# Kernel optimization log

Hardware: AMD Instinct MI355X
Metric: run time of the kernel (lower is better)

Reference implementation:

```python
import jax, jax.numpy as jnp
import numpy as np

N_QUBITS = 8
N_LAYERS = 2
BATCH = 16384
INPUT_DIM = 3072
NUM_CLASSES = 10

I2 = np.eye(2, dtype=np.complex64)
PAULIS = [
    I2,
    np.array([[0, 1], [1, 0]], np.complex64),      # X
    np.array([[0, -1j], [1j, 0]], np.complex64),   # Y
    np.array([[1, 0], [0, -1]], np.complex64),     # Z
]
XX = np.kron(PAULIS[1], PAULIS[1])
YY = np.kron(PAULIS[2], PAULIS[2])
ZZ = np.kron(PAULIS[3], PAULIS[3])
I4 = np.eye(4, dtype=np.complex64)


def u3(p):
    # PennyLane U3(theta, phi, lambda)
    th, ph, lam = p[0], p[1], p[2]
    c = jnp.cos(th / 2).astype(jnp.complex64)
    s = jnp.sin(th / 2).astype(jnp.complex64)
    return jnp.stack([
        jnp.stack([c, -jnp.exp(1j * lam) * s]),
        jnp.stack([jnp.exp(1j * ph) * s, jnp.exp(1j * (ph + lam)) * c]),
    ])


def cu3(p):
    U = u3(p)
    Z = jnp.zeros((2, 2), U.dtype)
    Ic = jnp.asarray(I2)
    top = jnp.concatenate([Ic, Z], axis=1)
    bot = jnp.concatenate([Z, U], axis=1)
    return jnp.concatenate([top, bot], axis=0)


def ising(P, phi):
    # exp(-i phi/2 * P) with P a 2-qubit Pauli word (P^2 = I)
    return jnp.cos(phi / 2) * I4 - 1j * jnp.sin(phi / 2) * P


def apply_1q(psi, U, w):
    psi = jnp.moveaxis(psi, 1 + w, -1)
    psi = jnp.einsum('ij,...j->...i', U, psi)
    return jnp.moveaxis(psi, -1, 1 + w)


def apply_2q(psi, U, a, b):
    psi = jnp.moveaxis(psi, (1 + a, 1 + b), (-2, -1))
    sh = psi.shape
    psi = jnp.einsum('ij,...j->...i', U, psi.reshape(sh[:-2] + (4,)))
    return jnp.moveaxis(psi.reshape(sh), (-2, -1), (1 + a, 1 + b))


def apply_ry_batched(psi, theta, w):
    # per-sample RY angle (AngleEmbedding, rotation='Y')
    c = jnp.cos(theta / 2).reshape((-1,) + (1,) * (psi.ndim - 2))
    s = jnp.sin(theta / 2).reshape((-1,) + (1,) * (psi.ndim - 2))
    psi = jnp.moveaxis(psi, 1 + w, -1)
    a0, a1 = psi[..., 0], psi[..., 1]
    psi = jnp.stack([c * a0 - s * a1, s * a0 + c * a1], axis=-1)
    return jnp.moveaxis(psi, -1, 1 + w)


def dilated_conv(psi, W, wires):
    n = len(wires)
    if n == 8:
        pairs = [(0, 2), (1, 3), (4, 6), (5, 7)]
    elif n == 4:
        pairs = [(0, 2), (1, 3)]
    elif n == 2:
        pairs = [(0, 1)]
    else:
        pairs = [(i, i + 2) for i in range(n - 2)]
    processed = set()
    for q1, q2 in pairs:
        if q1 in wires and q2 in wires:
            psi = apply_1q(psi, u3(W[q1, 0:3]), q1)
            psi = apply_1q(psi, u3(W[q2, 3:6]), q2)
            psi = apply_2q(psi, ising(ZZ, W[q1, 6]), q1, q2)
            psi = apply_2q(psi, ising(YY, W[q1, 7]), q1, q2)
            psi = apply_2q(psi, ising(XX, W[q1, 8]), q1, q2)
            psi = apply_1q(psi, u3(W[q1, 9:12]), q1)
            psi = apply_1q(psi, u3(W[q2, 12:15]), q2)
            processed.update((q1, q2))
    for w in wires:
        if w not in processed:
            for i in range(5):
                psi = apply_1q(psi, u3(W[w, 3 * i:3 * i + 3]), w)
    return psi


def pooling(psi, P, wires):
    for indx, w in enumerate(wires):
        if indx % 2 == 1:
            # measure wire w, cond-U3 on wires[indx-1]; deferred -> CU3(ctrl=w, tgt=wires[indx-1])
            psi = apply_2q(psi, cu3(P[indx // 2]), w, wires[indx - 1])
    return psi


def _gray_pauli_words(k):
    # matches pennylane _n_k_gray_code(4, k) ordering, identity word dropped
    words = []
    for i in range(4 ** k):
        br = []
        v = i
        for _ in range(k):
            br.append(v % 4)
            v //= 4
        cw = [0] * k
        shift = 0
        for j in reversed(range(k)):
            cw[j] = (br[j] + shift) % 4
            shift += 4 - cw[j]
        if any(cw):
            words.append(tuple(cw))
    return words


def arbitrary_unitary(psi, weights, wires):
    # qml.ArbitraryUnitary: sequence of PauliRot(weights[i], word) gates
    k = len(wires)
    Ik = np.eye(2 ** k, dtype=np.complex64)
    for idx, cw in enumerate(_gray_pauli_words(k)):
        P = np.array([[1.0]], np.complex64)
        for p in cw:
            P = np.kron(P, PAULIS[p])
        th = weights[idx]
        G = jnp.cos(th / 2) * Ik - 1j * jnp.sin(th / 2) * P
        psi = apply_2q(psi, G, wires[0], wires[1])
    return psi


def run_circuit(features, conv, pool, last):
    B = features.shape[0]
    psi = jnp.zeros((B, 2 ** N_QUBITS), jnp.complex64).at[:, 0].set(1.0)
    psi = psi.reshape((B,) + (2,) * N_QUBITS)
    for w in range(N_QUBITS):
        psi = apply_ry_batched(psi, features[:, w], w)
    wires = list(range(N_QUBITS))
    for layer in range(N_LAYERS):
        psi = dilated_conv(psi, conv[layer], wires)
        psi = pooling(psi, pool[layer], wires)
        wires = wires[::2]
    psi = arbitrary_unitary(psi, last, wires)
    probs = psi.real ** 2 + psi.imag ** 2
    z0 = probs[:, 0].reshape(B, -1).sum(-1) - probs[:, 1].reshape(B, -1).sum(-1)
    return z0  # <Z_0> per sample


def setup_inputs():
    key = jax.random.key(0)
    ks = jax.random.split(key, 8)
    return {
        'x': jax.random.normal(ks[0], (BATCH, INPUT_DIM), jnp.float32),
        'fc_w': jax.random.normal(ks[1], (N_QUBITS, INPUT_DIM), jnp.float32) * 0.02,
        'fc_b': jnp.zeros((N_QUBITS,), jnp.float32),
        'conv_params': jax.random.normal(ks[2], (N_LAYERS, N_QUBITS, 15), jnp.float32),
        'pool_params': jax.random.normal(ks[3], (N_LAYERS, N_QUBITS // 2, 3), jnp.float32),
        'last_params': jax.random.normal(ks[4], (15,), jnp.float32),
        'fc_out_w': jax.random.normal(ks[5], (NUM_CLASSES, 1), jnp.float32),
        'fc_out_b': jnp.zeros((NUM_CLASSES,), jnp.float32),
    }


def reference(x, fc_w, fc_b, conv_params, pool_params, last_params, fc_out_w, fc_out_b):
    reduced = jnp.tanh(x @ fc_w.T + fc_b)                      # (B, n_qubits)
    z0 = run_circuit(reduced, conv_params, pool_params, last_params)  # (B,)
    logits = z0[:, None] * fc_out_w[:, 0][None, :] + fc_out_b  # (B, num_classes)
    return logits
```

## Files before the change

### kernel.cpp

```cpp
#include <hip/hip_runtime.h>
#include <math.h>

__device__ inline float2 cmul(float2 a, float2 b){
  return make_float2(a.x*b.x - a.y*b.y, a.x*b.y + a.y*b.x);
}
__device__ inline void cfma(float2& acc, float2 a, float2 b){
  acc.x += a.x*b.x - a.y*b.y;
  acc.y += a.x*b.y + a.y*b.x;
}

__device__ inline void mk_u3(const float* p, float2& u00, float2& u01, float2& u10, float2& u11){
  float s, c;   sincosf(0.5f*p[0], &s, &c);
  float sl, cl; sincosf(p[1], &sl, &cl);
  float sm, cm; sincosf(p[2], &sm, &cm);
  float s2, c2; sincosf(p[1] + p[2], &s2, &c2);
  u00 = make_float2(c, 0.f);
  u01 = make_float2(-s*cm, -s*sm);
  u10 = make_float2( s*cl,  s*sl);
  u11 = make_float2( c*c2,  c*s2);
}

__device__ inline void pauli2(int t, float2* m){
  if (t == 0){ m[0]=make_float2(1,0); m[1]=make_float2(0,0);  m[2]=make_float2(0,0); m[3]=make_float2(1,0); }
  else if (t == 1){ m[0]=make_float2(0,0); m[1]=make_float2(1,0);  m[2]=make_float2(1,0); m[3]=make_float2(0,0); }
  else if (t == 2){ m[0]=make_float2(0,0); m[1]=make_float2(0,-1); m[2]=make_float2(0,1); m[3]=make_float2(0,0); }
  else            { m[0]=make_float2(1,0); m[1]=make_float2(0,0);  m[2]=make_float2(0,0); m[3]=make_float2(-1,0);}
}

struct GSpec { int type; int w1; int w2; int poff; };
#define NG 66
__device__ const GSpec gspec[NG] = {
  {0,0,0,  0},{0,2,0, 33},{1,0,2,  6},{2,0,2,  7},{3,0,2,  8},{0,0,0,  9},{0,2,0, 42},
  {0,1,0, 15},{0,3,0, 48},{1,1,3, 21},{2,1,3, 22},{3,1,3, 23},{0,1,0, 24},{0,3,0, 57},
  {0,4,0, 60},{0,6,0, 93},{1,4,6, 66},{2,4,6, 67},{3,4,6, 68},{0,4,0, 69},{0,6,0,102},
  {0,5,0, 75},{0,7,0,108},{1,5,7, 81},{2,5,7, 82},{3,5,7, 83},{0,5,0, 84},{0,7,0,117},
  {4,1,0,1000},{4,3,2,1003},{4,5,4,1006},{4,7,6,1009},
  {0,0,0,120},{0,2,0,153},{1,0,2,126},{2,0,2,127},{3,0,2,128},{0,0,0,129},{0,2,0,162},
  {0,4,0,180},{0,4,0,183},{0,4,0,186},{0,4,0,189},{0,4,0,192},
  {0,6,0,210},{0,6,0,213},{0,6,0,216},{0,6,0,219},{0,6,0,222},
  {4,2,0,1012},{4,6,4,1015},
  {5,1,0,2000},{5,2,0,2001},{5,3,0,2002},{5,3,1,2003},{5,0,1,2004},
  {5,1,1,2005},{5,2,1,2006},{5,2,2,2007},{5,3,2,2008},{5,0,2,2009},
  {5,1,2,2010},{5,1,3,2011},{5,2,3,2012},{5,3,3,2013},{5,0,3,2014},
};

__device__ inline void apply1q(float2* S, int lane, int bit,
                               float2 u00, float2 u01, float2 u10, float2 u11){
  #pragma unroll
  for (int t = 0; t < 2; t++){
    int p  = lane + 64*t;
    int k0 = ((p >> bit) << (bit+1)) | (p & ((1<<bit)-1));
    int k1 = k0 | (1 << bit);
    float2 a = S[k0], b = S[k1];
    float2 na = make_float2(u00.x*a.x - u00.y*a.y + u01.x*b.x - u01.y*b.y,
                            u00.x*a.y + u00.y*a.x + u01.x*b.y + u01.y*b.x);
    float2 nb = make_float2(u10.x*a.x - u10.y*a.y + u11.x*b.x - u11.y*b.y,
                            u10.x*a.y + u10.y*a.x + u11.x*b.y + u11.y*b.x);
    S[k0] = na; S[k1] = nb;
  }
  __syncthreads();
}

__device__ inline void apply2q(float2* S, int lane, int bitA, int bitB, const float2* G){
  int hi = bitA > bitB ? bitA : bitB;
  int lo = bitA ^ bitB ^ hi;
  int t2  = ((lane >> lo) << (lo+1)) | (lane & ((1<<lo)-1));
  int k00 = ((t2   >> hi) << (hi+1)) | (t2   & ((1<<hi)-1));
  int mA = 1 << bitA, mB = 1 << bitB;
  int id[4] = { k00, k00|mB, k00|mA, k00|mA|mB };
  float2 v[4];
  #pragma unroll
  for (int r = 0; r < 4; r++) v[r] = S[id[r]];
  #pragma unroll
  for (int r = 0; r < 4; r++){
    float re = 0.f, im = 0.f;
    #pragma unroll
    for (int c = 0; c < 4; c++){
      float2 g = G[r*4 + c];
      re += g.x*v[c].x - g.y*v[c].y;
      im += g.x*v[c].y + g.y*v[c].x;
    }
    S[id[r]] = make_float2(re, im);
  }
  __syncthreads();
}

__global__ __launch_bounds__(64) void kern_sim(const float* __restrict__ conv,
                                               const float* __restrict__ pool,
                                               const float* __restrict__ last,
                                               float2* __restrict__ U){
  __shared__ float2 Gt[NG*16];
  __shared__ float2 Ft[14*16];
  __shared__ float2 Ms[7*16];
  __shared__ float2 S[256];
  const int lane = threadIdx.x;
  const int j = blockIdx.x;

  for (int g = lane; g < NG; g += 64){
    GSpec sp = gspec[g];
    const float* base;
    if (sp.poff >= 2000)      base = last + (sp.poff - 2000);
    else if (sp.poff >= 1000) base = pool + (sp.poff - 1000);
    else                      base = conv + sp.poff;
    float2 G[16];
    #pragma unroll
    for (int i = 0; i < 16; i++) G[i] = make_float2(0.f, 0.f);
    if (sp.type == 0){
      float2 a,b,c,d; mk_u3(base,a,b,c,d);
      G[0]=a; G[1]=b; G[2]=c; G[3]=d;
    } else if (sp.type == 1){
      float s,co; sincosf(0.5f*base[0], &s, &co);
      G[0]=make_float2(co,-s); G[5]=make_float2(co,s); G[10]=make_float2(co,s); G[15]=make_float2(co,-s);
    } else if (sp.type == 2){
      float s,co; sincosf(0.5f*base[0], &s, &co);
      G[0]=G[5]=G[10]=G[15]=make_float2(co,0.f);
      G[3]=make_float2(0.f,s); G[6]=make_float2(0.f,-s); G[9]=make_float2(0.f,-s); G[12]=make_float2(0.f,s);
    } else if (sp.type == 3){
      float s,co; sincosf(0.5f*base[0], &s, &co);
      G[0]=G[5]=G[10]=G[15]=make_float2(co,0.f);
      G[3]=G[6]=G[9]=G[12]=make_float2(0.f,-s);
    } else if (sp.type == 4){
      float2 a,b,c,d; mk_u3(base,a,b,c,d);
      G[0]=make_float2(1.f,0.f); G[5]=make_float2(1.f,0.f);
      G[10]=a; G[11]=b; G[14]=c; G[15]=d;
    } else {
      float s,co; sincosf(0.5f*base[0], &s, &co);
      float2 A2[4], B2[4]; pauli2(sp.w1,A2); pauli2(sp.w2,B2);
      #pragma unroll
      for (int i1 = 0; i1 < 2; i1++)
      #pragma unroll
      for (int i2 = 0; i2 < 2; i2++)
      #pragma unroll
      for (int j1 = 0; j1 < 2; j1++)
      #pragma unroll
      for (int j2 = 0; j2 < 2; j2++){
        float2 Pv = cmul(A2[i1*2+j1], B2[i2*2+j2]);
        int rr = i1*2+i2, cc = j1*2+j2;
        G[rr*4+cc] = make_float2((rr==cc ? co : 0.f) + s*Pv.y, -s*Pv.x);
      }
    }
    #pragma unroll
    for (int i = 0; i < 16; i++) Gt[g*16 + i] = G[i];
  }
  __syncthreads();

  const int fe = lane & 15;
  const int fr = fe >> 2, fc = fe & 3;

  {
    const int p  = lane >> 4;
    const int gb = p*7;
    float2 va = Gt[gb*16     + (fr>>1)*2 + (fc>>1)];
    float2 vb = Gt[(gb+1)*16 + (fr&1)*2  + (fc&1)];
    Ms[p*16 + fe] = cmul(va, vb);
    __syncthreads();
    for (int s = 0; s < 3; s++){
      float2 acc = make_float2(0.f, 0.f);
      #pragma unroll
      for (int k = 0; k < 4; k++)
        cfma(acc, Gt[(gb+2+s)*16 + fr*4 + k], Ms[p*16 + k*4 + fc]);
      __syncthreads();
      Ms[p*16 + fe] = acc;
      __syncthreads();
    }
    float2 ka = Gt[(gb+5)*16 + (fr>>1)*2 + (fc>>1)];
    float2 kb = Gt[(gb+6)*16 + (fr&1)*2  + (fc&1)];
    Ft[p*16 + fe] = cmul(ka, kb);
    __syncthreads();
    float2 acc = make_float2(0.f, 0.f);
    #pragma unroll
    for (int k = 0; k < 4; k++)
      cfma(acc, Ft[p*16 + fr*4 + k], Ms[p*16 + k*4 + fc]);
    __syncthreads();
    Ft[p*16 + fe] = acc;
    __syncthreads();
  }

  {
    const int grp = lane >> 4;
    if (grp == 0){
      float2 va = Gt[32*16 + (fr>>1)*2 + (fc>>1)];
      float2 vb = Gt[33*16 + (fr&1)*2  + (fc&1)];
      Ms[4*16 + fe] = cmul(va, vb);
    } else if (grp == 1){
      Ms[5*16 + fe] = Gt[51*16 + fe];
    } else if (lane < 40){
      int t = (lane-32)>>2, e2 = (lane-32)&3;
      Ms[6*16 + t*4 + e2] = Gt[(39+5*t)*16 + e2];
    }
    __syncthreads();
    for (int s = 1; s <= 14; s++){
      float2 val = make_float2(0.f, 0.f);
      int wf = 0, dst = 0;
      if (grp == 0){
        if (s <= 3){
          #pragma unroll
          for (int k = 0; k < 4; k++)
            cfma(val, Gt[(33+s)*16 + fr*4 + k], Ms[4*16 + k*4 + fc]);
          wf = 1; dst = 4*16 + fe;
        } else if (s == 4){
          float2 ka = Gt[37*16 + (fr>>1)*2 + (fc>>1)];
          float2 kb = Gt[38*16 + (fr&1)*2  + (fc&1)];
          val = cmul(ka, kb); wf = 1; dst = 0*16 + fe;
        } else if (s == 5){
          #pragma unroll
          for (int k = 0; k < 4; k++)
            cfma(val, Ms[0*16 + fr*4 + k], Ms[4*16 + k*4 + fc]);
          wf = 2; dst = 4*16 + fe;
        }
      } else if (grp == 1){
        #pragma unroll
        for (int k = 0; k < 4; k++)
          cfma(val, Gt[(51+s)*16 + fr*4 + k], Ms[5*16 + k*4 + fc]);
        if (s == 14){ wf = 2; dst = 13*16 + fe; }
        else        { wf = 1; dst = 5*16 + fe; }
      } else if (lane < 40 && s <= 4){
        int t = (lane-32)>>2, e2 = (lane-32)&3, r2 = e2>>1, c2 = e2&1;
        #pragma unroll
        for (int k = 0; k < 2; k++)
          cfma(val, Gt[(39+5*t+s)*16 + r2*2 + k], Ms[6*16 + t*4 + k*2 + c2]);
        if (s == 4){ wf = 2; dst = (5+t)*16 + e2; }
        else       { wf = 1; dst = 6*16 + t*4 + e2; }
      }
      __syncthreads();
      if (wf == 1) Ms[dst] = val;
      else if (wf == 2) Ft[dst] = val;
      __syncthreads();
    }
    for (int idx = lane; idx < 96; idx += 64){
      int q = idx >> 4, e = idx & 15;
      int gid = (q < 4) ? (28+q) : (q == 4 ? 49 : 50);
      Ft[(7+q)*16 + e] = Gt[gid*16 + e];
    }
  }
  __syncthreads();

  #pragma unroll
  for (int t = 0; t < 4; t++){ int k = lane + 64*t; S[k] = make_float2(k==j ? 1.f : 0.f, 0.f); }
  __syncthreads();

  apply2q(S, lane, 7, 5, &Ft[0*16]);
  apply2q(S, lane, 6, 4, &Ft[1*16]);
  apply2q(S, lane, 3, 1, &Ft[2*16]);
  apply2q(S, lane, 2, 0, &Ft[3*16]);
  apply2q(S, lane, 6, 7, &Ft[7*16]);
  apply2q(S, lane, 4, 5, &Ft[8*16]);
  apply2q(S, lane, 2, 3, &Ft[9*16]);
  apply2q(S, lane, 0, 1, &Ft[10*16]);
  apply2q(S, lane, 7, 5, &Ft[4*16]);
  apply1q(S, lane, 3, Ft[5*16+0], Ft[5*16+1], Ft[5*16+2], Ft[5*16+3]);
  apply1q(S, lane, 1, Ft[6*16+0], Ft[6*16+1], Ft[6*16+2], Ft[6*16+3]);
  apply2q(S, lane, 5, 7, &Ft[11*16]);
  apply2q(S, lane, 1, 3, &Ft[12*16]);
  apply2q(S, lane, 7, 3, &Ft[13*16]);

  #pragma unroll
  for (int t = 0; t < 4; t++){ int k = lane + 64*t; U[k*256 + j] = S[k]; }
}

__global__ __launch_bounds__(256) void kern_m2(const float2* __restrict__ U,
                                               float* __restrict__ mt){
  __shared__ float dsh[256];
  const int xm = blockIdx.x, i = threadIdx.x;
  const int j2 = i ^ xm;
  float acc = 0.f;
  #pragma unroll 4
  for (int k = 0; k < 128; k++){
    float2 ui0 = U[k*256 + i];
    float2 uj0 = U[k*256 + j2];
    float2 ui1 = U[(k+128)*256 + i];
    float2 uj1 = U[(k+128)*256 + j2];
    acc += (ui0.x*uj0.x + ui0.y*uj0.y) - (ui1.x*uj1.x + ui1.y*uj1.y);
  }
  dsh[i] = acc;
  __syncthreads();
  for (int bit = 1; bit < 256; bit <<= 1){
    float mine = dsh[i], other = dsh[i ^ bit];
    __syncthreads();
    dsh[i] = (i & bit) ? (other - mine) : (mine + other);
    __syncthreads();
  }
  if ((i & xm) == 0){
    int idx = 0, pw = 1;
    #pragma unroll
    for (int b2 = 0; b2 < 8; b2++){
      int dg = ((xm >> b2) & 1) ? 1 : (((i >> b2) & 1) ? 2 : 0);
      idx += dg * pw; pw *= 3;
    }
    mt[idx] = dsh[i] * (1.0f/256.0f);
  }
}

__global__ __launch_bounds__(256) void kern_gemv(const float* __restrict__ x,
                                                 const float* __restrict__ w,
                                                 const float* __restrict__ b,
                                                 float* __restrict__ red){
  __shared__ float4 wl[1536];
  const int tid = threadIdx.x;
  const int wave = tid >> 6, lane = tid & 63;
  const int rl = lane >> 5, co = lane & 31;
  const int row0 = blockIdx.x*16 + wave*4 + rl*2;
  const float4* xp0 = (const float4*)(x + (size_t)row0*3072);
  const float4* xp1 = (const float4*)(x + (size_t)(row0+1)*3072);
  const float4* wp  = (const float4*)w;
  float accA[8], accB[8];
  #pragma unroll
  for (int q = 0; q < 8; q++){ accA[q] = 0.f; accB[q] = 0.f; }

  for (int qt = 0; qt < 4; qt++){
    __syncthreads();
    #pragma unroll
    for (int i = 0; i < 6; i++){
      int idx = tid + 256*i;
      int q = idx / 192, cc = idx - q*192;
      wl[idx] = wp[q*768 + qt*192 + cc];
    }
    __syncthreads();
    #pragma unroll
    for (int it = 0; it < 6; it++){
      int cl = it*32 + co;
      float4 xa = xp0[qt*192 + cl];
      float4 xb = xp1[qt*192 + cl];
      #pragma unroll
      for (int q = 0; q < 8; q++){
        float4 wv = wl[q*192 + cl];
        accA[q] += wv.x*xa.x + wv.y*xa.y + wv.z*xa.z + wv.w*xa.w;
        accB[q] += wv.x*xb.x + wv.y*xb.y + wv.z*xb.z + wv.w*xb.w;
      }
    }
  }

  #pragma unroll
  for (int q = 0; q < 8; q++){
    float va = accA[q], vb = accB[q];
    va += __shfl_xor(va, 1);  vb += __shfl_xor(vb, 1);
    va += __shfl_xor(va, 2);  vb += __shfl_xor(vb, 2);
    va += __shfl_xor(va, 4);  vb += __shfl_xor(vb, 4);
    va += __shfl_xor(va, 8);  vb += __shfl_xor(vb, 8);
    va += __shfl_xor(va, 16); vb += __shfl_xor(vb, 16);
    accA[q] = va; accB[q] = vb;
  }
  if (co == 0){
    float4 a0 = make_float4(tanhf(accA[0]+b[0]), tanhf(accA[1]+b[1]),
                            tanhf(accA[2]+b[2]), tanhf(accA[3]+b[3]));
    float4 a1 = make_float4(tanhf(accA[4]+b[4]), tanhf(accA[5]+b[5]),
                            tanhf(accA[6]+b[6]), tanhf(accA[7]+b[7]));
    float4* rpA = (float4*)(red + (size_t)row0*8);
    rpA[0] = a0; rpA[1] = a1;
    float4 b0 = make_float4(tanhf(accB[0]+b[0]), tanhf(accB[1]+b[1]),
                            tanhf(accB[2]+b[2]), tanhf(accB[3]+b[3]));
    float4 b1 = make_float4(tanhf(accB[4]+b[4]), tanhf(accB[5]+b[5]),
                            tanhf(accB[6]+b[6]), tanhf(accB[7]+b[7]));
    float4* rpB = (float4*)(red + (size_t)(row0+1)*8);
    rpB[0] = b0; rpB[1] = b1;
  }
}

__global__ __launch_bounds__(256) void kern_contract(const float* __restrict__ red,
                                                     const float* __restrict__ mt,
                                                     const float* __restrict__ fow,
                                                     const float* __restrict__ fob,
                                                     float* __restrict__ out){
  __shared__ float mtl[9*27*32];
  __shared__ float zsh[4*64];
  const int tid = threadIdx.x;
  for (int idx = tid; idx < 9*27*32; idx += 256){
    int h  = idx / 864;
    int r  = idx - h*864;
    int mm = r >> 5, l = r & 31;
    mtl[idx] = (l < 27) ? mt[h*729 + mm*27 + l] : 0.f;
  }
  const int wave = tid >> 6, lane = tid & 63;
  const int e = blockIdx.x*64 + lane;
  const float4* rp = (const float4*)(red + (size_t)e*8);
  float4 r0 = rp[0], r1 = rp[1];
  __syncthreads();

  float rr[8] = {r0.x, r0.y, r0.z, r0.w, r1.x, r1.y, r1.z, r1.w};
  float sn[8], cs[8];
  #pragma unroll
  for (int q = 0; q < 8; q++) sincosf(rr[q], &sn[q], &cs[q]);
  float f0[3] = {1.f, sn[7], cs[7]};
  float f1[3] = {1.f, sn[6], cs[6]};
  float f2[3] = {1.f, sn[5], cs[5]};
  float g27[32];
  #pragma unroll
  for (int z = 27; z < 32; z++) g27[z] = 0.f;
  #pragma unroll
  for (int d2 = 0; d2 < 3; d2++)
  #pragma unroll
  for (int d1 = 0; d1 < 3; d1++)
  #pragma unroll
  for (int d0 = 0; d0 < 3; d0++)
    g27[9*d2 + 3*d1 + d0] = f2[d2]*f1[d1]*f0[d0];
  float4 glo4[8];
  #pragma unroll
  for (int v = 0; v < 8; v++)
    glo4[v] = make_float4(g27[4*v], g27[4*v+1], g27[4*v+2], g27[4*v+3]);
  float f3[3] = {1.f, sn[4], cs[4]};
  float f4[3] = {1.f, sn[3], cs[3]};
  float f5[3] = {1.f, sn[2], cs[2]};
  float gmid[27];
  #pragma unroll
  for (int d5 = 0; d5 < 3; d5++)
  #pragma unroll
  for (int d4 = 0; d4 < 3; d4++)
  #pragma unroll
  for (int d3 = 0; d3 < 3; d3++)
    gmid[9*d5 + 3*d4 + d3] = f5[d5]*f4[d4]*f3[d3];
  float f6[3] = {1.f, sn[1], cs[1]};
  float f7[3] = {1.f, sn[0], cs[0]};
  float ghi[9];
  #pragma unroll
  for (int d7 = 0; d7 < 3; d7++)
  #pragma unroll
  for (int d6 = 0; d6 < 3; d6++)
    ghi[3*d7 + d6] = f7[d7]*f6[d6];

  const int hbeg = (wave==0) ? 0 : (wave==1) ? 3 : (wave==2) ? 5 : 7;
  const int hend = hbeg + ((wave==0) ? 3 : 2);
  float part = 0.f;
  for (int h = hbeg; h < hend; h++){
    float ha = 0.f, hb = 0.f;
    #pragma unroll 3
    for (int mm = 0; mm < 27; mm++){
      const float4* mp = (const float4*)&mtl[(h*27 + mm) << 5];
      float d0 = 0.f, d1 = 0.f;
      #pragma unroll
      for (int v = 0; v < 8; v += 2){
        float4 m0 = mp[v], m1 = mp[v+1];
        d0 += m0.x*glo4[v].x   + m0.y*glo4[v].y   + m0.z*glo4[v].z   + m0.w*glo4[v].w;
        d1 += m1.x*glo4[v+1].x + m1.y*glo4[v+1].y + m1.z*glo4[v+1].z + m1.w*glo4[v+1].w;
      }
      float term = (d0 + d1) * gmid[mm];
      if (mm & 1) hb += term; else ha += term;
    }
    part += (ha + hb) * ghi[h];
  }
  zsh[wave*64 + lane] = part;
  __syncthreads();

  for (int idx = tid; idx < 640; idx += 256){
    int el = idx / 10, c = idx - el*10;
    float z = zsh[el] + zsh[64+el] + zsh[128+el] + zsh[192+el];
    out[((size_t)blockIdx.x*64 + el)*10 + c] = z*fow[c] + fob[c];
  }
}

extern "C" void kernel_launch(void* const* d_in, const int* in_sizes, int n_in,
                              void* d_out, int out_size, void* d_ws, size_t ws_size,
                              hipStream_t stream) {
  (void)in_sizes; (void)n_in; (void)out_size; (void)ws_size;
  const float* x    = (const float*)d_in[0];
  const float* fcw  = (const float*)d_in[1];
  const float* fcb  = (const float*)d_in[2];
  const float* conv = (const float*)d_in[3];
  const float* pool = (const float*)d_in[4];
  const float* last = (const float*)d_in[5];
  const float* fow  = (const float*)d_in[6];
  const float* fob  = (const float*)d_in[7];
  float* out = (float*)d_out;

  char* ws = (char*)d_ws;
  float2* U   = (float2*)ws;
  float*  red = (float*) (ws + 512*1024);
  float*  mt  = (float*) (ws + 1024*1024);

  kern_sim     <<<256,  64,  0, stream>>>(conv, pool, last, U);
  kern_m2      <<<256,  256, 0, stream>>>(U, mt);
  kern_gemv    <<<1024, 256, 0, stream>>>(x, fcw, fcb, red);
  kern_contract<<<256,  256, 0, stream>>>(red, mt, fow, fob, out);
}
```

Baseline: 355.8 us.

## Fuse circuit simulation into GEMV launch and pad mt layout in global memory

Merges the GEMV kernel and the unitary-simulation kernel into one launch. Blocks 0-1023 run the FC reduction and blocks 1024+ simulate circuit columns with 256 threads, the extra threads idling during gate application. kern_m2 now writes the moment tensor directly in the padded 32-stride layout and zeroes the padding. kern_contract then reads it straight from global/L2 instead of staging it in shared memory. The intent is to remove one launch, overlap the small sim work with the bandwidth-bound GEMV, and cut the per-block shared-memory staging in the contraction. The cost is that the sim blocks become less efficient and the contraction loads go through the cache.

```diff
diff --git a/kernel.cpp b/kernel.cpp
--- a/kernel.cpp
+++ b/kernel.cpp
@@ -44,11 +44,10 @@
   {5,1,2,2010},{5,1,3,2011},{5,2,3,2012},{5,3,3,2013},{5,0,3,2014},
 };
 
-__device__ inline void apply1q(float2* S, int lane, int bit,
-                               float2 u00, float2 u01, float2 u10, float2 u11){
-  #pragma unroll
-  for (int t = 0; t < 2; t++){
-    int p  = lane + 64*t;
+__device__ inline void apply1q_b(float2* S, int tid, int bit,
+                                 float2 u00, float2 u01, float2 u10, float2 u11){
+  if (tid < 128){
+    int p  = tid;
     int k0 = ((p >> bit) << (bit+1)) | (p & ((1<<bit)-1));
     int k1 = k0 | (1 << bit);
     float2 a = S[k0], b = S[k1];
@@ -61,42 +60,113 @@
   __syncthreads();
 }
 
-__device__ inline void apply2q(float2* S, int lane, int bitA, int bitB, const float2* G){
-  int hi = bitA > bitB ? bitA : bitB;
-  int lo = bitA ^ bitB ^ hi;
-  int t2  = ((lane >> lo) << (lo+1)) | (lane & ((1<<lo)-1));
-  int k00 = ((t2   >> hi) << (hi+1)) | (t2   & ((1<<hi)-1));
-  int mA = 1 << bitA, mB = 1 << bitB;
-  int id[4] = { k00, k00|mB, k00|mA, k00|mA|mB };
-  float2 v[4];
-  #pragma unroll
-  for (int r = 0; r < 4; r++) v[r] = S[id[r]];
-  #pragma unroll
-  for (int r = 0; r < 4; r++){
-    float re = 0.f, im = 0.f;
-    #pragma unroll
-    for (int c = 0; c < 4; c++){
-      float2 g = G[r*4 + c];
-      re += g.x*v[c].x - g.y*v[c].y;
-      im += g.x*v[c].y + g.y*v[c].x;
-    }
-    S[id[r]] = make_float2(re, im);
-  }
-  __syncthreads();
-}
-
-__global__ __launch_bounds__(64) void kern_sim(const float* __restrict__ conv,
-                                               const float* __restrict__ pool,
-                                               const float* __restrict__ last,
-                                               float2* __restrict__ U){
-  __shared__ float2 Gt[NG*16];
-  __shared__ float2 Ft[14*16];
-  __shared__ float2 Ms[7*16];
-  __shared__ float2 S[256];
-  const int lane = threadIdx.x;
-  const int j = blockIdx.x;
-
-  for (int g = lane; g < NG; g += 64){
+__device__ inline void apply2q_b(float2* S, int tid, int bitA, int bitB, const float2* G){
+  if (tid < 64){
+    int lane = tid;
+    int hi = bitA > bitB ? bitA : bitB;
+    int lo = bitA ^ bitB ^ hi;
+    int t2  = ((lane >> lo) << (lo+1)) | (lane & ((1<<lo)-1));
+    int k00 = ((t2   >> hi) << (hi+1)) | (t2   & ((1<<hi)-1));
+    int mA = 1 << bitA, mB = 1 << bitB;
+    int id[4] = { k00, k00|mB, k00|mA, k00|mA|mB };
+    float2 v[4];
+    #pragma unroll
+    for (int r = 0; r < 4; r++) v[r] = S[id[r]];
+    #pragma unroll
+    for (int r = 0; r < 4; r++){
+      float re = 0.f, im = 0.f;
+      #pragma unroll
+      for (int c = 0; c < 4; c++){
+        float2 g = G[r*4 + c];
+        re += g.x*v[c].x - g.y*v[c].y;
+        im += g.x*v[c].y + g.y*v[c].x;
+      }
+      S[id[r]] = make_float2(re, im);
+    }
+  }
+  __syncthreads();
+}
+
+__global__ __launch_bounds__(256) void kern_a(const float* __restrict__ x,
+                                              const float* __restrict__ w,
+                                              const float* __restrict__ b,
+                                              const float* __restrict__ conv,
+                                              const float* __restrict__ pool,
+                                              const float* __restrict__ last,
+                                              float* __restrict__ red,
+                                              float2* __restrict__ U){
+  __shared__ float4 smem4[1536];
+  const int tid = threadIdx.x;
+
+  if (blockIdx.x < 1024){
+    float4* wl = smem4;
+    const int wave = tid >> 6, lane = tid & 63;
+    const int rl = lane >> 5, co = lane & 31;
+    const int row0 = blockIdx.x*16 + wave*4 + rl*2;
+    const float4* xp0 = (const float4*)(x + (size_t)row0*3072);
+    const float4* xp1 = (const float4*)(x + (size_t)(row0+1)*3072);
+    const float4* wp  = (const float4*)w;
+    float accA[8], accB[8];
+    #pragma unroll
+    for (int q = 0; q < 8; q++){ accA[q] = 0.f; accB[q] = 0.f; }
+
+    for (int qt = 0; qt < 4; qt++){
+      __syncthreads();
+      #pragma unroll
+      for (int i = 0; i < 6; i++){
+        int idx = tid + 256*i;
+        int q = idx / 192, cc = idx - q*192;
+        wl[idx] = wp[q*768 + qt*192 + cc];
+      }
+      __syncthreads();
+      #pragma unroll
+      for (int it = 0; it < 6; it++){
+        int cl = it*32 + co;
+        float4 xa = xp0[qt*192 + cl];
+        float4 xb = xp1[qt*192 + cl];
+        #pragma unroll
+        for (int q = 0; q < 8; q++){
+          float4 wv = wl[q*192 + cl];
+          accA[q] += wv.x*xa.x + wv.y*xa.y + wv.z*xa.z + wv.w*xa.w;
+          accB[q] += wv.x*xb.x + wv.y*xb.y + wv.z*xb.z + wv.w*xb.w;
+        }
+      }
+    }
+
+    #pragma unroll
+    for (int q = 0; q < 8; q++){
+      float va = accA[q], vb = accB[q];
+      va += __shfl_xor(va, 1);  vb += __shfl_xor(vb, 1);
+      va += __shfl_xor(va, 2);  vb += __shfl_xor(vb, 2);
+      va += __shfl_xor(va, 4);  vb += __shfl_xor(vb, 4);
+      va += __shfl_xor(va, 8);  vb += __shfl_xor(vb, 8);
+      va += __shfl_xor(va, 16); vb += __shfl_xor(vb, 16);
+      accA[q] = va; accB[q] = vb;
+    }
+    if (co == 0){
+      float4 a0 = make_float4(tanhf(accA[0]+b[0]), tanhf(accA[1]+b[1]),
+                              tanhf(accA[2]+b[2]), tanhf(accA[3]+b[3]));
+      float4 a1 = make_float4(tanhf(accA[4]+b[4]), tanhf(accA[5]+b[5]),
+                              tanhf(accA[6]+b[6]), tanhf(accA[7]+b[7]));
+      float4* rpA = (float4*)(red + (size_t)row0*8);
+      rpA[0] = a0; rpA[1] = a1;
+      float4 b0 = make_float4(tanhf(accB[0]+b[0]), tanhf(accB[1]+b[1]),
+                              tanhf(accB[2]+b[2]), tanhf(accB[3]+b[3]));
+      float4 b1 = make_float4(tanhf(accB[4]+b[4]), tanhf(accB[5]+b[5]),
+                              tanhf(accB[6]+b[6]), tanhf(accB[7]+b[7]));
+      float4* rpB = (float4*)(red + (size_t)(row0+1)*8);
+      rpB[0] = b0; rpB[1] = b1;
+    }
+    return;
+  }
+
+  const int j = blockIdx.x - 1024;
+  float2* Gt = (float2*)smem4;
+  float2* Ft = Gt + NG*16;
+  float2* Ms = Ft + 14*16;
+  float2* S  = Ms + 7*16;
+
+  for (int g = tid; g < NG; g += 256){
     GSpec sp = gspec[g];
     const float* base;
     if (sp.poff >= 2000)      base = last + (sp.poff - 2000);
@@ -106,8 +176,8 @@
     #pragma unroll
     for (int i = 0; i < 16; i++) G[i] = make_float2(0.f, 0.f);
     if (sp.type == 0){
-      float2 a,b,c,d; mk_u3(base,a,b,c,d);
-      G[0]=a; G[1]=b; G[2]=c; G[3]=d;
+      float2 a,bb,c,d; mk_u3(base,a,bb,c,d);
+      G[0]=a; G[1]=bb; G[2]=c; G[3]=d;
     } else if (sp.type == 1){
       float s,co; sincosf(0.5f*base[0], &s, &co);
       G[0]=make_float2(co,-s); G[5]=make_float2(co,s); G[10]=make_float2(co,s); G[15]=make_float2(co,-s);
@@ -120,9 +190,9 @@
       G[0]=G[5]=G[10]=G[15]=make_float2(co,0.f);
       G[3]=G[6]=G[9]=G[12]=make_float2(0.f,-s);
     } else if (sp.type == 4){
-      float2 a,b,c,d; mk_u3(base,a,b,c,d);
+      float2 a,bb,c,d; mk_u3(base,a,bb,c,d);
       G[0]=make_float2(1.f,0.f); G[5]=make_float2(1.f,0.f);
-      G[10]=a; G[11]=b; G[14]=c; G[15]=d;
+      G[10]=a; G[11]=bb; G[14]=c; G[15]=d;
     } else {
       float s,co; sincosf(0.5f*base[0], &s, &co);
       float2 A2[4], B2[4]; pauli2(sp.w1,A2); pauli2(sp.w2,B2);
@@ -144,48 +214,57 @@
   }
   __syncthreads();
 
-  const int fe = lane & 15;
+  const int fe = tid & 15;
   const int fr = fe >> 2, fc = fe & 3;
 
   {
-    const int p  = lane >> 4;
+    const bool act = tid < 64;
+    const int p  = tid >> 4;
     const int gb = p*7;
-    float2 va = Gt[gb*16     + (fr>>1)*2 + (fc>>1)];
-    float2 vb = Gt[(gb+1)*16 + (fr&1)*2  + (fc&1)];
-    Ms[p*16 + fe] = cmul(va, vb);
+    if (act){
+      float2 va = Gt[gb*16     + (fr>>1)*2 + (fc>>1)];
+      float2 vb = Gt[(gb+1)*16 + (fr&1)*2  + (fc&1)];
+      Ms[p*16 + fe] = cmul(va, vb);
+    }
     __syncthreads();
     for (int s = 0; s < 3; s++){
       float2 acc = make_float2(0.f, 0.f);
+      if (act){
+        #pragma unroll
+        for (int k = 0; k < 4; k++)
+          cfma(acc, Gt[(gb+2+s)*16 + fr*4 + k], Ms[p*16 + k*4 + fc]);
+      }
+      __syncthreads();
+      if (act) Ms[p*16 + fe] = acc;
+      __syncthreads();
+    }
+    if (act){
+      float2 ka = Gt[(gb+5)*16 + (fr>>1)*2 + (fc>>1)];
+      float2 kb = Gt[(gb+6)*16 + (fr&1)*2  + (fc&1)];
+      Ft[p*16 + fe] = cmul(ka, kb);
+    }
+    __syncthreads();
+    float2 acc2 = make_float2(0.f, 0.f);
+    if (act){
       #pragma unroll
       for (int k = 0; k < 4; k++)
-        cfma(acc, Gt[(gb+2+s)*16 + fr*4 + k], Ms[p*16 + k*4 + fc]);
-      __syncthreads();
-      Ms[p*16 + fe] = acc;
-      __syncthreads();
-    }
-    float2 ka = Gt[(gb+5)*16 + (fr>>1)*2 + (fc>>1)];
-    float2 kb = Gt[(gb+6)*16 + (fr&1)*2  + (fc&1)];
-    Ft[p*16 + fe] = cmul(ka, kb);
-    __syncthreads();
-    float2 acc = make_float2(0.f, 0.f);
-    #pragma unroll
-    for (int k = 0; k < 4; k++)
-      cfma(acc, Ft[p*16 + fr*4 + k], Ms[p*16 + k*4 + fc]);
-    __syncthreads();
-    Ft[p*16 + fe] = acc;
+        cfma(acc2, Ft[p*16 + fr*4 + k], Ms[p*16 + k*4 + fc]);
+    }
+    __syncthreads();
+    if (act) Ft[p*16 + fe] = acc2;
     __syncthreads();
   }
 
   {
-    const int grp = lane >> 4;
+    const int grp = tid >> 4;
     if (grp == 0){
       float2 va = Gt[32*16 + (fr>>1)*2 + (fc>>1)];
       float2 vb = Gt[33*16 + (fr&1)*2  + (fc&1)];
       Ms[4*16 + fe] = cmul(va, vb);
     } else if (grp == 1){
       Ms[5*16 + fe] = Gt[51*16 + fe];
-    } else if (lane < 40){
-      int t = (lane-32)>>2, e2 = (lane-32)&3;
+    } else if (tid < 40){
+      int t = (tid-32)>>2, e2 = (tid-32)&3;
       Ms[6*16 + t*4 + e2] = Gt[(39+5*t)*16 + e2];
     }
     __syncthreads();
@@ -214,8 +293,8 @@
           cfma(val, Gt[(51+s)*16 + fr*4 + k], Ms[5*16 + k*4 + fc]);
         if (s == 14){ wf = 2; dst = 13*16 + fe; }
         else        { wf = 1; dst = 5*16 + fe; }
-      } else if (lane < 40 && s <= 4){
-        int t = (lane-32)>>2, e2 = (lane-32)&3, r2 = e2>>1, c2 = e2&1;
+      } else if (tid < 40 && s <= 4){
+        int t = (tid-32)>>2, e2 = (tid-32)&3, r2 = e2>>1, c2 = e2&1;
         #pragma unroll
         for (int k = 0; k < 2; k++)
           cfma(val, Gt[(39+5*t+s)*16 + r2*2 + k], Ms[6*16 + t*4 + k*2 + c2]);
@@ -227,7 +306,7 @@
       else if (wf == 2) Ft[dst] = val;
       __syncthreads();
     }
-    for (int idx = lane; idx < 96; idx += 64){
+    for (int idx = tid; idx < 96; idx += 256){
       int q = idx >> 4, e = idx & 15;
       int gid = (q < 4) ? (28+q) : (q == 4 ? 49 : 50);
       Ft[(7+q)*16 + e] = Gt[gid*16 + e];
@@ -235,33 +314,37 @@
   }
   __syncthreads();
 
-  #pragma unroll
-  for (int t = 0; t < 4; t++){ int k = lane + 64*t; S[k] = make_float2(k==j ? 1.f : 0.f, 0.f); }
-  __syncthreads();
-
-  apply2q(S, lane, 7, 5, &Ft[0*16]);
-  apply2q(S, lane, 6, 4, &Ft[1*16]);
-  apply2q(S, lane, 3, 1, &Ft[2*16]);
-  apply2q(S, lane, 2, 0, &Ft[3*16]);
-  apply2q(S, lane, 6, 7, &Ft[7*16]);
-  apply2q(S, lane, 4, 5, &Ft[8*16]);
-  apply2q(S, lane, 2, 3, &Ft[9*16]);
-  apply2q(S, lane, 0, 1, &Ft[10*16]);
-  apply2q(S, lane, 7, 5, &Ft[4*16]);
-  apply1q(S, lane, 3, Ft[5*16+0], Ft[5*16+1], Ft[5*16+2], Ft[5*16+3]);
-  apply1q(S, lane, 1, Ft[6*16+0], Ft[6*16+1], Ft[6*16+2], Ft[6*16+3]);
-  apply2q(S, lane, 5, 7, &Ft[11*16]);
-  apply2q(S, lane, 1, 3, &Ft[12*16]);
-  apply2q(S, lane, 7, 3, &Ft[13*16]);
-
-  #pragma unroll
-  for (int t = 0; t < 4; t++){ int k = lane + 64*t; U[k*256 + j] = S[k]; }
+  S[tid] = make_float2(tid==j ? 1.f : 0.f, 0.f);
+  __syncthreads();
+
+  apply2q_b(S, tid, 7, 5, &Ft[0*16]);
+  apply2q_b(S, tid, 6, 4, &Ft[1*16]);
+  apply2q_b(S, tid, 3, 1, &Ft[2*16]);
+  apply2q_b(S, tid, 2, 0, &Ft[3*16]);
+  apply2q_b(S, tid, 6, 7, &Ft[7*16]);
+  apply2q_b(S, tid, 4, 5, &Ft[8*16]);
+  apply2q_b(S, tid, 2, 3, &Ft[9*16]);
+  apply2q_b(S, tid, 0, 1, &Ft[10*16]);
+  apply2q_b(S, tid, 7, 5, &Ft[4*16]);
+  apply1q_b(S, tid, 3, Ft[5*16+0], Ft[5*16+1], Ft[5*16+2], Ft[5*16+3]);
+  apply1q_b(S, tid, 1, Ft[6*16+0], Ft[6*16+1], Ft[6*16+2], Ft[6*16+3]);
+  apply2q_b(S, tid, 5, 7, &Ft[11*16]);
+  apply2q_b(S, tid, 1, 3, &Ft[12*16]);
+  apply2q_b(S, tid, 7, 3, &Ft[13*16]);
+
+  U[tid*256 + j] = S[tid];
 }
 
 __global__ __launch_bounds__(256) void kern_m2(const float2* __restrict__ U,
                                                float* __restrict__ mt){
   __shared__ float dsh[256];
   const int xm = blockIdx.x, i = threadIdx.x;
+  if (xm == 0){
+    for (int z = i; z < 1215; z += 256){
+      int hm = z/5, l = z - hm*5;
+      mt[hm*32 + 27 + l] = 0.f;
+    }
+  }
   const int j2 = i ^ xm;
   float acc = 0.f;
   #pragma unroll 4
@@ -281,78 +364,15 @@
     __syncthreads();
   }
   if ((i & xm) == 0){
-    int idx = 0, pw = 1;
+    int idx = 0;
     #pragma unroll
     for (int b2 = 0; b2 < 8; b2++){
+      const int w8 = (b2==0)?1:(b2==1)?3:(b2==2)?9:(b2==3)?32:
+                     (b2==4)?96:(b2==5)?288:(b2==6)?864:2592;
       int dg = ((xm >> b2) & 1) ? 1 : (((i >> b2) & 1) ? 2 : 0);
-      idx += dg * pw; pw *= 3;
+      idx += dg * w8;
     }
     mt[idx] = dsh[i] * (1.0f/256.0f);
-  }
-}
-
-__global__ __launch_bounds__(256) void kern_gemv(const float* __restrict__ x,
-                                                 const float* __restrict__ w,
-                                                 const float* __restrict__ b,
-                                                 float* __restrict__ red){
-  __shared__ float4 wl[1536];
-  const int tid = threadIdx.x;
-  const int wave = tid >> 6, lane = tid & 63;
-  const int rl = lane >> 5, co = lane & 31;
-  const int row0 = blockIdx.x*16 + wave*4 + rl*2;
-  const float4* xp0 = (const float4*)(x + (size_t)row0*3072);
-  const float4* xp1 = (const float4*)(x + (size_t)(row0+1)*3072);
-  const float4* wp  = (const float4*)w;
-  float accA[8], accB[8];
-  #pragma unroll
-  for (int q = 0; q < 8; q++){ accA[q] = 0.f; accB[q] = 0.f; }
-
-  for (int qt = 0; qt < 4; qt++){
-    __syncthreads();
-    #pragma unroll
-    for (int i = 0; i < 6; i++){
-      int idx = tid + 256*i;
-      int q = idx / 192, cc = idx - q*192;
-      wl[idx] = wp[q*768 + qt*192 + cc];
-    }
-    __syncthreads();
-    #pragma unroll
-    for (int it = 0; it < 6; it++){
-      int cl = it*32 + co;
-      float4 xa = xp0[qt*192 + cl];
-      float4 xb = xp1[qt*192 + cl];
-      #pragma unroll
-      for (int q = 0; q < 8; q++){
-        float4 wv = wl[q*192 + cl];
-        accA[q] += wv.x*xa.x + wv.y*xa.y + wv.z*xa.z + wv.w*xa.w;
-        accB[q] += wv.x*xb.x + wv.y*xb.y + wv.z*xb.z + wv.w*xb.w;
-      }
-    }
-  }
-
-  #pragma unroll
-  for (int q = 0; q < 8; q++){
-    float va = accA[q], vb = accB[q];
-    va += __shfl_xor(va, 1);  vb += __shfl_xor(vb, 1);
-    va += __shfl_xor(va, 2);  vb += __shfl_xor(vb, 2);
-    va += __shfl_xor(va, 4);  vb += __shfl_xor(vb, 4);
-    va += __shfl_xor(va, 8);  vb += __shfl_xor(vb, 8);
-    va += __shfl_xor(va, 16); vb += __shfl_xor(vb, 16);
-    accA[q] = va; accB[q] = vb;
-  }
-  if (co == 0){
-    float4 a0 = make_float4(tanhf(accA[0]+b[0]), tanhf(accA[1]+b[1]),
-                            tanhf(accA[2]+b[2]), tanhf(accA[3]+b[3]));
-    float4 a1 = make_float4(tanhf(accA[4]+b[4]), tanhf(accA[5]+b[5]),
-                            tanhf(accA[6]+b[6]), tanhf(accA[7]+b[7]));
-    float4* rpA = (float4*)(red + (size_t)row0*8);
-    rpA[0] = a0; rpA[1] = a1;
-    float4 b0 = make_float4(tanhf(accB[0]+b[0]), tanhf(accB[1]+b[1]),
-                            tanhf(accB[2]+b[2]), tanhf(accB[3]+b[3]));
-    float4 b1 = make_float4(tanhf(accB[4]+b[4]), tanhf(accB[5]+b[5]),
-                            tanhf(accB[6]+b[6]), tanhf(accB[7]+b[7]));
-    float4* rpB = (float4*)(red + (size_t)(row0+1)*8);
-    rpB[0] = b0; rpB[1] = b1;
   }
 }
 
@@ -361,20 +381,12 @@
                                                      const float* __restrict__ fow,
                                                      const float* __restrict__ fob,
                                                      float* __restrict__ out){
-  __shared__ float mtl[9*27*32];
   __shared__ float zsh[4*64];
   const int tid = threadIdx.x;
-  for (int idx = tid; idx < 9*27*32; idx += 256){
-    int h  = idx / 864;
-    int r  = idx - h*864;
-    int mm = r >> 5, l = r & 31;
-    mtl[idx] = (l < 27) ? mt[h*729 + mm*27 + l] : 0.f;
-  }
   const int wave = tid >> 6, lane = tid & 63;
   const int e = blockIdx.x*64 + lane;
   const float4* rp = (const float4*)(red + (size_t)e*8);
   float4 r0 = rp[0], r1 = rp[1];
-  __syncthreads();
 
   float rr[8] = {r0.x, r0.y, r0.z, r0.w, r1.x, r1.y, r1.z, r1.w};
   float sn[8], cs[8];
@@ -424,7 +436,7 @@
     float ha = 0.f, hb = 0.f;
     #pragma unroll 3
     for (int mm = 0; mm < 27; mm++){
-      const float4* mp = (const float4*)&mtl[(h*27 + mm) << 5];
+      const float4* mp = (const float4*)(mt + (size_t)((h*27 + mm) << 5));
       float d0 = 0.f, d1 = 0.f;
       #pragma unroll
       for (int v = 0; v < 8; v += 2){
@@ -466,8 +478,7 @@
   float*  red = (float*) (ws + 512*1024);
   float*  mt  = (float*) (ws + 1024*1024);
 
-  kern_sim     <<<256,  64,  0, stream>>>(conv, pool, last, U);
+  kern_a       <<<1280, 256, 0, stream>>>(x, fcw, fcb, conv, pool, last, red, U);
   kern_m2      <<<256,  256, 0, stream>>>(U, mt);
-  kern_gemv    <<<1024, 256, 0, stream>>>(x, fcw, fcb, red);
   kern_contract<<<256,  256, 0, stream>>>(red, mt, fow, fob, out);
 }
```

Result: slower. 364.6 us (+2.5%).
